# Performance work log

Measured on AMD Instinct MI355X. Metric: run time of the kernel, lower is better.

Reference implementation:

```python
import jax, jax.numpy as jnp
import numpy as np

BODY = 10      # inds_objs[0][0]
FEAT = 15      # len(inds_objs[0])
NOBJ = 8
HALF = 130     # dimo // 2
B = 65536


def _obj_idx():
    # column indices for each object's features: [NOBJ, 2*FEAT]
    base = BODY + FEAT * np.arange(NOBJ)[:, None] + np.arange(FEAT)[None, :]  # [NOBJ, FEAT]
    return jnp.asarray(np.concatenate([base, base + HALF], axis=1))           # [NOBJ, 30]


def setup_inputs() -> dict:
    key = jax.random.key(0)
    ks = jax.random.split(key, 9)
    def w(k, shape):
        fan_in = shape[0]
        return jax.random.normal(k, shape, jnp.float32) * (1.0 / np.sqrt(fan_in))
    return {
        "o": jax.random.normal(ks[0], (B, 260), jnp.float32),
        "g": jax.random.normal(ks[1], (B, 100), jnp.float32),
        "W_cast": w(ks[2], (100, 50)), "b_cast": jnp.zeros((50,), jnp.float32),
        "W_a0": w(ks[3], (50, 256)),   "b_a0": jnp.zeros((256,), jnp.float32),
        "W_a1": w(ks[4], (256, 400)),  "b_a1": jnp.zeros((400,), jnp.float32),
        "W_p0": w(ks[5], (400, 256)),  "b_p0": jnp.zeros((256,), jnp.float32),
        "W_p1": w(ks[6], (256, 256)),  "b_p1": jnp.zeros((256,), jnp.float32),
        "W_p2": w(ks[7], (256, 8)),    "b_p2": jnp.zeros((8,), jnp.float32),
    }


def reference(o, g, W_cast, b_cast, W_a0, b_a0, W_a1, b_a1,
              W_p0, b_p0, W_p1, b_p1, W_p2, b_p2):
    # attention gate from goal encoding: [B, 50]
    attention = jax.nn.sigmoid(g @ W_cast + b_cast)
    # body features (pos + vel halves): [B, 20]
    obs_body = jnp.concatenate([o[:, :BODY], o[:, HALF:HALF + BODY]], axis=1)
    # per-object features gathered in one shot: [B, NOBJ, 30]
    obs_obj = o[:, _obj_idx()]
    # concat body with each object: [B, NOBJ, 50]
    x = jnp.concatenate(
        [jnp.broadcast_to(obs_body[:, None, :], (o.shape[0], NOBJ, 2 * BODY)), obs_obj],
        axis=2)
    # elementwise attention gate (shared across objects)
    x = x * attention[:, None, :]
    # fc_actor: 50 -> 256 (relu) -> 400, then extra relu from forward()
    h = jax.nn.relu(jnp.einsum('bnd,dh->bnh', x, W_a0) + b_a0)
    y = jax.nn.relu(jnp.einsum('bnh,hk->bnk', h, W_a1) + b_a1)
    # deepset sum over objects: [B, 400]
    input_pi = y.sum(axis=1)
    # fc_pi: 400 -> 256 (relu) -> 256 (relu) -> 8, then tanh
    p = jax.nn.relu(input_pi @ W_p0 + b_p0)
    p = jax.nn.relu(p @ W_p1 + b_p1)
    return jnp.tanh(p @ W_p2 + b_p2)
```

## Files before the change

kernel.cpp:

```cpp
#include <hip/hip_runtime.h>
#include <hip/hip_bf16.h>

typedef _Float16 f16;
typedef f16 v8h __attribute__((ext_vector_type(8)));
typedef float v4f __attribute__((ext_vector_type(4)));
typedef float v2f __attribute__((ext_vector_type(2)));
typedef unsigned short u16;
typedef unsigned int u32;

__device__ __forceinline__ u16 f2h(float f) {
  f16 h = (f16)f;
  return __builtin_bit_cast(unsigned short, h);
}
__device__ __forceinline__ float h2f(u16 u) {
  f16 h = __builtin_bit_cast(f16, u);
  return (float)h;
}
#define MFMA16(a, b, c) __builtin_amdgcn_mfma_f32_16x16x32_f16((a), (b), (c), 0, 0, 0)

__global__ void prep_weights(const float* __restrict__ Wc, const float* __restrict__ Wa0,
                             const float* __restrict__ Wa1, const float* __restrict__ Wp0,
                             const float* __restrict__ Wp1, const float* __restrict__ Wp2,
                             u16* __restrict__ ws) {
  int idx = blockIdx.x * 256 + threadIdx.x;
  float v;
  if (idx < 8192) {
    int n = idx >> 7, k = idx & 127;
    v = (n < 50 && k < 100) ? Wc[k * 50 + n] : 0.f;
  } else if (idx < 24576) {
    int i = idx - 8192; int n = i >> 6, k = i & 63;
    v = (k < 50) ? Wa0[k * 256 + n] : 0.f;
  } else if (idx < 126976) {
    int i = idx - 24576; int n = i >> 8, k = i & 255;
    v = Wa1[k * 400 + n];
  } else if (idx < 233472) {
    int i = idx - 126976; int n = i / 416, k = i - n * 416;
    v = (k < 400) ? Wp0[k * 256 + n] : 0.f;
  } else if (idx < 299008) {
    int i = idx - 233472; int n = i >> 8, k = i & 255;
    v = Wp1[k * 256 + n];
  } else if (idx < 303104) {
    int i = idx - 299008; int n = i >> 8, k = i & 255;
    v = (n < 8) ? Wp2[k * 8 + n] : 0.f;
  } else {
    return;
  }
  ws[idx] = f2h(v);
}

__global__ __launch_bounds__(1024) void actor_kernel(
    const float* __restrict__ o, const float* __restrict__ g,
    const float* __restrict__ b_cast, const float* __restrict__ b_a0,
    const float* __restrict__ b_a1, const float* __restrict__ b_p0,
    const float* __restrict__ b_p1, const float* __restrict__ b_p2,
    const u16* __restrict__ wsb, float* __restrict__ out) {
  __shared__ __align__(16) char smem[148480];
  u16* sAtt = (u16*)smem;
  u16* sG   = (u16*)(smem + 7168);
  u16* sX0  = (u16*)(smem + 7168);
  u16* sH0  = (u16*)(smem + 80896);
  u16* sH1  = (u16*)(smem + 114688);
  u16* sY   = (u16*)(smem + 7168);
  u16* sP   = (u16*)(smem + 7168);

  const u16* WcT  = wsb;
  const u16* Wa0T = wsb + 8192;
  const u16* Wa1T = wsb + 24576;
  const u16* Wp0T = wsb + 126976;
  const u16* Wp1T = wsb + 233472;
  const u16* Wp2T = wsb + 299008;

  const int tid  = threadIdx.x;
  const int lane = tid & 63;
  const int w    = tid >> 6;
  const int nl   = lane & 15;
  const int q    = lane >> 4;
  const int row0 = blockIdx.x * 64;

  for (int idx = tid; idx < 64 * 128; idx += 1024) {
    int r = idx >> 7, c = idx & 127;
    float v = (c < 100) ? __builtin_nontemporal_load(&g[(size_t)(row0 + r) * 100 + c]) : 0.f;
    sG[r * 136 + c] = f2h(v);
  }
  __syncthreads();

  {
    const int rb = w >> 2, nbq = w & 3;
    const int col = nbq * 16 + nl;
    v4f acc = {};
#pragma unroll
    for (int kb = 0; kb < 4; ++kb) {
      v8h bh = *(const v8h*)(WcT + col * 128 + kb * 32 + q * 8);
      v8h a  = *(const v8h*)&sG[(rb * 16 + nl) * 136 + kb * 32 + q * 8];
      acc = MFMA16(a, bh, acc);
    }
    if (col < 50) {
      float bias = b_cast[col];
#pragma unroll
      for (int rg = 0; rg < 4; ++rg) {
        float v = acc[rg] + bias;
        v = 1.f / (1.f + __expf(-v));
        sAtt[(rb * 16 + q * 4 + rg) * 56 + col] = f2h(v);
      }
    }
  }
  __syncthreads();

#pragma unroll
  for (int i = 0; i < 4; ++i) {
    int idx = tid + i * 1024;
    if (idx < 3840) {
      int r = idx / 60, c2 = idx - r * 60;
      const float* rp = o + (size_t)(row0 + r) * 260;
      v2f f1 = *(const v2f*)(rp + 10 + 2 * c2);
      v2f f2 = *(const v2f*)(rp + 140 + 2 * c2);
      int cc0 = 2 * c2, cc1 = cc0 + 1;
      int ob0 = cc0 / 15, j0 = cc0 - ob0 * 15;
      int ob1 = cc1 / 15, j1 = cc1 - ob1 * 15;
      u16* xr = sX0 + r * 72;
      xr[ob0 * 4608 + 20 + j0] = f2h(f1[0] * h2f(sAtt[r * 56 + 20 + j0]));
      xr[ob1 * 4608 + 20 + j1] = f2h(f1[1] * h2f(sAtt[r * 56 + 20 + j1]));
      xr[ob0 * 4608 + 35 + j0] = f2h(f2[0] * h2f(sAtt[r * 56 + 35 + j0]));
      xr[ob1 * 4608 + 35 + j1] = f2h(f2[1] * h2f(sAtt[r * 56 + 35 + j1]));
    }
  }
  if (tid < 640) {
    int r = tid / 10, hh = tid - r * 10;
    const float* rp = o + (size_t)(row0 + r) * 260;
    int src = (hh < 5) ? (2 * hh) : (2 * hh + 120);
    v2f fb = *(const v2f*)(rp + src);
    int c0 = 2 * hh, c1 = c0 + 1;
    u16 x0 = f2h(fb[0] * h2f(sAtt[r * 56 + c0]));
    u16 x1 = f2h(fb[1] * h2f(sAtt[r * 56 + c1]));
    u16* xr = sX0 + r * 72;
#pragma unroll
    for (int ob = 0; ob < 8; ++ob) {
      xr[ob * 4608 + c0] = x0;
      xr[ob * 4608 + c1] = x1;
    }
  }
  for (int idx = tid; idx < 64 * 8 * 7; idx += 1024) {
    int t = idx; int uu = t % 7; t /= 7; int ob = t & 7; int r = t >> 3;
    *(u32*)&sX0[ob * 4608 + r * 72 + 50 + 2 * uu] = 0;
  }
  __syncthreads();

  const int  nb0  = w;
  const int  nb1  = w + 16;
  const bool has1 = (nb1 < 25);
  v4f y0[4] = {};
  v4f y1[4] = {};

  for (int obj = 0; obj < 8; ++obj) {
    u16* sHd = (obj & 1) ? sH1 : sH0;
    const u16* sXo = sX0 + obj * 4608;

    {
      v4f acc[4] = {};
#pragma unroll
      for (int kb = 0; kb < 2; ++kb) {
        v8h b0 = *(const v8h*)(Wa0T + (w * 16 + nl) * 64 + kb * 32 + q * 8);
#pragma unroll
        for (int rb = 0; rb < 4; ++rb) {
          v8h a = *(const v8h*)&sXo[(rb * 16 + nl) * 72 + kb * 32 + q * 8];
          acc[rb] = MFMA16(a, b0, acc[rb]);
        }
      }
      const int col = w * 16 + nl;
      float bias = b_a0[col];
#pragma unroll
      for (int rb = 0; rb < 4; ++rb)
#pragma unroll
        for (int rg = 0; rg < 4; ++rg) {
          float v = acc[rb][rg] + bias;
          v = v > 0.f ? v : 0.f;
          sHd[(rb * 16 + q * 4 + rg) * 264 + col] = f2h(v);
        }
    }
    __syncthreads();

    {
      v4f t0[4] = {}, t1[4] = {};
#pragma unroll
      for (int kb = 0; kb < 8; ++kb) {
        v8h b0 = *(const v8h*)(Wa1T + (nb0 * 16 + nl) * 256 + kb * 32 + q * 8);
        v8h b1;
        if (has1) b1 = *(const v8h*)(Wa1T + (nb1 * 16 + nl) * 256 + kb * 32 + q * 8);
#pragma unroll
        for (int rb = 0; rb < 4; ++rb) {
          v8h a = *(const v8h*)&sHd[(rb * 16 + nl) * 264 + kb * 32 + q * 8];
          t0[rb] = MFMA16(a, b0, t0[rb]);
          if (has1) t1[rb] = MFMA16(a, b1, t1[rb]);
        }
      }
      float bias0 = b_a1[nb0 * 16 + nl];
#pragma unroll
      for (int rb = 0; rb < 4; ++rb)
#pragma unroll
        for (int rg = 0; rg < 4; ++rg) {
          float v = t0[rb][rg] + bias0;
          y0[rb][rg] += (v > 0.f ? v : 0.f);
        }
      if (has1) {
        float bias1 = b_a1[nb1 * 16 + nl];
#pragma unroll
        for (int rb = 0; rb < 4; ++rb)
#pragma unroll
          for (int rg = 0; rg < 4; ++rg) {
            float v = t1[rb][rg] + bias1;
            y1[rb][rg] += (v > 0.f ? v : 0.f);
          }
      }
    }
  }
  __syncthreads();

  for (int idx = tid; idx < 64 * 16; idx += 1024) {
    int r = idx >> 4, c = idx & 15;
    sY[r * 424 + 400 + c] = 0;
  }
#pragma unroll
  for (int rb = 0; rb < 4; ++rb)
#pragma unroll
    for (int rg = 0; rg < 4; ++rg) {
      const int row = rb * 16 + q * 4 + rg;
      sY[row * 424 + nb0 * 16 + nl] = f2h(y0[rb][rg]);
      if (has1) sY[row * 424 + nb1 * 16 + nl] = f2h(y1[rb][rg]);
    }
  __syncthreads();

  v4f p0acc[4] = {};
#pragma unroll
  for (int kb = 0; kb < 13; ++kb) {
    v8h b0 = *(const v8h*)(Wp0T + (w * 16 + nl) * 416 + kb * 32 + q * 8);
#pragma unroll
    for (int rb = 0; rb < 4; ++rb) {
      v8h a = *(const v8h*)&sY[(rb * 16 + nl) * 424 + kb * 32 + q * 8];
      p0acc[rb] = MFMA16(a, b0, p0acc[rb]);
    }
  }
  __syncthreads();
  {
    const int col = w * 16 + nl;
    float bias = b_p0[col];
#pragma unroll
    for (int rb = 0; rb < 4; ++rb)
#pragma unroll
      for (int rg = 0; rg < 4; ++rg) {
        float v = p0acc[rb][rg] + bias;
        v = v > 0.f ? v : 0.f;
        sP[(rb * 16 + q * 4 + rg) * 264 + col] = f2h(v);
      }
  }
  __syncthreads();

  v4f p1acc[4] = {};
#pragma unroll
  for (int kb = 0; kb < 8; ++kb) {
    v8h b0 = *(const v8h*)(Wp1T + (w * 16 + nl) * 256 + kb * 32 + q * 8);
#pragma unroll
    for (int rb = 0; rb < 4; ++rb) {
      v8h a = *(const v8h*)&sP[(rb * 16 + nl) * 264 + kb * 32 + q * 8];
      p1acc[rb] = MFMA16(a, b0, p1acc[rb]);
    }
  }
  __syncthreads();
  {
    const int col = w * 16 + nl;
    float bias = b_p1[col];
#pragma unroll
    for (int rb = 0; rb < 4; ++rb)
#pragma unroll
      for (int rg = 0; rg < 4; ++rg) {
        float v = p1acc[rb][rg] + bias;
        v = v > 0.f ? v : 0.f;
        sP[(rb * 16 + q * 4 + rg) * 264 + col] = f2h(v);
      }
  }
  __syncthreads();

  if (w < 4) {
    v4f acc = {};
#pragma unroll
    for (int kb = 0; kb < 8; ++kb) {
      v8h a = *(const v8h*)&sP[(w * 16 + nl) * 264 + kb * 32 + q * 8];
      v8h b = *(const v8h*)(Wp2T + nl * 256 + kb * 32 + q * 8);
      acc = MFMA16(a, b, acc);
    }
    if (nl < 8) {
      float bias = b_p2[nl];
#pragma unroll
      for (int rg = 0; rg < 4; ++rg)
        __builtin_nontemporal_store(tanhf(acc[rg] + bias),
                                    &out[(size_t)(row0 + w * 16 + q * 4 + rg) * 8 + nl]);
    }
  }
}

extern "C" void kernel_launch(void* const* d_in, const int* in_sizes, int n_in,
                              void* d_out, int out_size, void* d_ws, size_t ws_size,
                              hipStream_t stream) {
  const float* o   = (const float*)d_in[0];
  const float* g   = (const float*)d_in[1];
  const float* Wc  = (const float*)d_in[2];
  const float* bc  = (const float*)d_in[3];
  const float* Wa0 = (const float*)d_in[4];
  const float* ba0 = (const float*)d_in[5];
  const float* Wa1 = (const float*)d_in[6];
  const float* ba1 = (const float*)d_in[7];
  const float* Wp0 = (const float*)d_in[8];
  const float* bp0 = (const float*)d_in[9];
  const float* Wp1 = (const float*)d_in[10];
  const float* bp1 = (const float*)d_in[11];
  const float* Wp2 = (const float*)d_in[12];
  const float* bp2 = (const float*)d_in[13];
  u16* ws = (u16*)d_ws;
  float* out = (float*)d_out;

  int rows = in_sizes[0] / 260;

  prep_weights<<<1184, 256, 0, stream>>>(Wc, Wa0, Wa1, Wp0, Wp1, Wp2, ws);
  actor_kernel<<<rows / 64, 1024, 0, stream>>>(o, g, bc, ba0, ba1, bp0, bp1, bp2, ws, out);
}
```

Measured before the change: 341.9 us.

## Software-pipeline layer-0 of next object with layer-1 of current object

```diff
diff --git a/kernel.cpp b/kernel.cpp
--- a/kernel.cpp
+++ b/kernel.cpp
@@ -151,11 +151,36 @@
   v4f y0[4] = {};
   v4f y1[4] = {};
 
+  {
+    v4f acc[4] = {};
+#pragma unroll
+    for (int kb = 0; kb < 2; ++kb) {
+      v8h b0 = *(const v8h*)(Wa0T + (w * 16 + nl) * 64 + kb * 32 + q * 8);
+#pragma unroll
+      for (int rb = 0; rb < 4; ++rb) {
+        v8h a = *(const v8h*)&sX0[(rb * 16 + nl) * 72 + kb * 32 + q * 8];
+        acc[rb] = MFMA16(a, b0, acc[rb]);
+      }
+    }
+    const int col = w * 16 + nl;
+    float bias = b_a0[col];
+#pragma unroll
+    for (int rb = 0; rb < 4; ++rb)
+#pragma unroll
+      for (int rg = 0; rg < 4; ++rg) {
+        float v = acc[rb][rg] + bias;
+        v = v > 0.f ? v : 0.f;
+        sH0[(rb * 16 + q * 4 + rg) * 264 + col] = f2h(v);
+      }
+  }
+  __syncthreads();
+
   for (int obj = 0; obj < 8; ++obj) {
-    u16* sHd = (obj & 1) ? sH1 : sH0;
-    const u16* sXo = sX0 + obj * 4608;
-
-    {
+    u16* bufCur  = (obj & 1) ? sH1 : sH0;
+    u16* bufNext = (obj & 1) ? sH0 : sH1;
+
+    if (obj < 7) {
+      const u16* sXo = sX0 + (obj + 1) * 4608;
       v4f acc[4] = {};
 #pragma unroll
       for (int kb = 0; kb < 2; ++kb) {
@@ -174,10 +199,9 @@
         for (int rg = 0; rg < 4; ++rg) {
           float v = acc[rb][rg] + bias;
           v = v > 0.f ? v : 0.f;
-          sHd[(rb * 16 + q * 4 + rg) * 264 + col] = f2h(v);
+          bufNext[(rb * 16 + q * 4 + rg) * 264 + col] = f2h(v);
         }
     }
-    __syncthreads();
 
     {
       v4f t0[4] = {}, t1[4] = {};
@@ -188,7 +212,7 @@
         if (has1) b1 = *(const v8h*)(Wa1T + (nb1 * 16 + nl) * 256 + kb * 32 + q * 8);
 #pragma unroll
         for (int rb = 0; rb < 4; ++rb) {
-          v8h a = *(const v8h*)&sHd[(rb * 16 + nl) * 264 + kb * 32 + q * 8];
+          v8h a = *(const v8h*)&bufCur[(rb * 16 + nl) * 264 + kb * 32 + q * 8];
           t0[rb] = MFMA16(a, b0, t0[rb]);
           if (has1) t1[rb] = MFMA16(a, b1, t1[rb]);
         }
@@ -212,8 +236,8 @@
           }
       }
     }
-  }
-  __syncthreads();
+    __syncthreads();
+  }
 
   for (int idx = tid; idx < 64 * 16; idx += 1024) {
     int r = idx >> 4, c = idx & 15;
```

Measured after the change: 369.8 us. +8.2%, slower.
